# Optimization experiments

Hardware: AMD Instinct MI355X
Metric: run time of the kernel (lower is better)

The kernel has to match this reference:

```python
import jax, jax.numpy as jnp
import numpy as np

N_NODES = 100000
IN_CH, HID_CH, OUT_CH = 128, 256, 128
N_EDGES = 1600000


def setup_inputs() -> dict:
    key = jax.random.key(0)
    k_x, k_e, k_w1, k_b1, k_w2, k_b2 = jax.random.split(key, 6)
    x = jax.random.normal(k_x, (N_NODES, IN_CH), dtype=jnp.float32)
    edge_index = jax.random.randint(k_e, (2, N_EDGES), 0, N_NODES, dtype=jnp.int64)
    # MLP params (Linear stores weight [out,in]; we keep [in,out] for x @ W)
    lim1 = 1.0 / np.sqrt(IN_CH)
    lim2 = 1.0 / np.sqrt(HID_CH)
    W1 = jax.random.uniform(k_w1, (IN_CH, HID_CH), jnp.float32, -lim1, lim1)
    b1 = jax.random.uniform(k_b1, (HID_CH,), jnp.float32, -lim1, lim1)
    W2 = jax.random.uniform(k_w2, (HID_CH, OUT_CH), jnp.float32, -lim2, lim2)
    b2 = jax.random.uniform(k_b2, (OUT_CH,), jnp.float32, -lim2, lim2)
    eps = jnp.zeros((), jnp.float32)  # train_eps=True, init 0
    return {"x": x, "edge_index": edge_index, "W1": W1, "b1": b1,
            "W2": W2, "b2": b2, "eps": eps}


def reference(x, edge_index, W1, b1, W2, b2, eps):
    src, dst = edge_index[0], edge_index[1]
    # scatter-add neighbor aggregation: aggr[i] = sum_{(j->i)} x[j]
    aggr = jax.ops.segment_sum(x[src], dst, num_segments=N_NODES)  # [N, in]
    h = (1.0 + eps) * x + aggr
    h = jax.nn.relu(h @ W1 + b1)
    h = h @ W2 + b2
    h = jax.nn.relu(h)
    # dropout is identity in eval mode
    return jax.nn.log_softmax(h, axis=-1)
```

## Files before the change

### kernel.cpp

```cpp
#include <hip/hip_runtime.h>

#define N_NODES 100000
#define IN_CH 128
#define HID_CH 256
#define OUT_CH 128
#define N_EDGES 1600000

#define NBK 782
#define BIN_BLOCKS 256
#define EPB (N_EDGES / BIN_BLOCKS)

typedef __attribute__((ext_vector_type(8))) short short8;
typedef __attribute__((ext_vector_type(4))) float f32x4;

__device__ __forceinline__ float b2f(ushort u) {
    unsigned int x = ((unsigned int)u) << 16;
    return __uint_as_float(x);
}
__device__ __forceinline__ ushort f2b(float f) {
    unsigned int u = __float_as_uint(f);
    u += 0x7FFFu + ((u >> 16) & 1u);
    return (ushort)(u >> 16);
}

#define PREP_X_BLOCKS 6250
#define PREP_W1_BLOCKS 128
#define PREP_W2_BLOCKS 128
#define PREP_TOTAL (PREP_X_BLOCKS + PREP_W1_BLOCKS + PREP_W2_BLOCKS)
__global__ __launch_bounds__(256) void prep_kernel(
    const float* __restrict__ x, const float* __restrict__ W1,
    const float* __restrict__ W2, const int* __restrict__ dst,
    ushort* __restrict__ xb, ushort* __restrict__ W1T,
    ushort* __restrict__ W2T, int* __restrict__ histT) {
    const int b = blockIdx.x;
    const int t = threadIdx.x;
    if (b < PREP_X_BLOCKS) {
        const size_t i = (size_t)b * 2048 + t * 8;
        float4 a = *reinterpret_cast<const float4*>(x + i);
        float4 c = *reinterpret_cast<const float4*>(x + i + 4);
        ushort v[8] = {f2b(a.x), f2b(a.y), f2b(a.z), f2b(a.w),
                       f2b(c.x), f2b(c.y), f2b(c.z), f2b(c.w)};
        *reinterpret_cast<short8*>(xb + i) = *reinterpret_cast<short8*>(v);
    } else if (b < PREP_X_BLOCKS + PREP_W1_BLOCKS) {
        const int i = (b - PREP_X_BLOCKS) * 256 + t;
        const int oc = i >> 7, k = i & 127;
        W1T[i] = f2b(W1[k * HID_CH + oc]);
    } else if (b < PREP_TOTAL) {
        const int i = (b - PREP_X_BLOCKS - PREP_W1_BLOCKS) * 256 + t;
        const int oc = i >> 8, k = i & 255;
        W2T[i] = f2b(W2[k * OUT_CH + oc]);
    } else {
        __shared__ int h[NBK];
        const int bb = b - PREP_TOTAL;
        for (int k = t; k < NBK; k += 256) h[k] = 0;
        __syncthreads();
        const int base = bb * EPB;
        for (int i = t; i < EPB; i += 256)
            atomicAdd(&h[dst[base + i] >> 7], 1);
        __syncthreads();
        for (int k = t; k < NBK; k += 256) histT[k * BIN_BLOCKS + bb] = h[k];
    }
}

__global__ __launch_bounds__(256) void scanA_kernel(
    const int* __restrict__ histT, int* __restrict__ blockBaseP,
    int* __restrict__ bktTotal) {
    __shared__ int ts[256];
    const int bk = blockIdx.x, t = threadIdx.x;
    const int v = histT[bk * BIN_BLOCKS + t];
    ts[t] = v;
    __syncthreads();
    #pragma unroll
    for (int o = 1; o < 256; o <<= 1) {
        int add = (t >= o) ? ts[t - o] : 0;
        __syncthreads();
        ts[t] += add;
        __syncthreads();
    }
    blockBaseP[bk * BIN_BLOCKS + t] = ts[t] - v;
    if (t == 255) bktTotal[bk] = ts[255];
}

__global__ __launch_bounds__(1024) void scanB_kernel(
    const int* __restrict__ bktTotal, int* __restrict__ bktBase) {
    __shared__ int ts[1024];
    const int t = threadIdx.x;
    const int v = (t < NBK) ? bktTotal[t] : 0;
    ts[t] = v;
    __syncthreads();
    #pragma unroll
    for (int o = 1; o < 1024; o <<= 1) {
        int add = (t >= o) ? ts[t - o] : 0;
        __syncthreads();
        ts[t] += add;
        __syncthreads();
    }
    if (t < NBK) bktBase[t] = ts[t] - v;
}

__global__ __launch_bounds__(256) void bin_kernel(
    const int* __restrict__ src, const int* __restrict__ dst,
    const int* __restrict__ blockBaseP, const int* __restrict__ bktBase,
    unsigned int* __restrict__ ebuf) {
    __shared__ int base[NBK];
    __shared__ int cur[NBK];
    const int b = blockIdx.x, t = threadIdx.x;
    for (int k = t; k < NBK; k += 256) {
        base[k] = bktBase[k] + blockBaseP[k * BIN_BLOCKS + b];
        cur[k] = 0;
    }
    __syncthreads();
    const int ebase = b * EPB;
    for (int i = t; i < EPB; i += 256) {
        const int d = dst[ebase + i];
        const int s = src[ebase + i];
        const int bk = d >> 7;
        const int r = atomicAdd(&cur[bk], 1);
        ebuf[base[bk] + r] = ((unsigned int)(d & 127) << 17) | (unsigned int)s;
    }
}

__global__ __launch_bounds__(256) void group_kernel(
    const unsigned int* __restrict__ ebuf,
    const int* __restrict__ bktBase, const int* __restrict__ bktTotal,
    int* __restrict__ csr_src, int* __restrict__ offs) {
    __shared__ int hist[128];
    __shared__ int cur[128];
    const int bk = blockIdx.x, t = threadIdx.x;
    if (t < 128) hist[t] = 0;
    __syncthreads();
    const int start = bktBase[bk];
    const int cnt   = bktTotal[bk];
    for (int i = t; i < cnt; i += 256)
        atomicAdd(&hist[ebuf[start + i] >> 17], 1);
    __syncthreads();
    int v = (t < 128) ? hist[t] : 0;
    #pragma unroll
    for (int o = 1; o < 128; o <<= 1) {
        int add = (t < 128 && t >= o) ? hist[t - o] : 0;
        __syncthreads();
        if (t < 128) hist[t] += add;
        __syncthreads();
    }
    if (t < 128) {
        const int excl = hist[t] - v;
        cur[t] = excl;
        const int node = bk * 128 + t;
        if (node < N_NODES) offs[node] = start + excl;
    }
    if (bk == 0 && t == 0) offs[N_NODES] = N_EDGES;
    __syncthreads();
    for (int i = t; i < cnt; i += 256) {
        const unsigned int e = ebuf[start + i];
        const int dl = e >> 17;
        const int p = atomicAdd(&cur[dl], 1);
        csr_src[start + p] = (int)(e & 0x1FFFF);
    }
}

__global__ __launch_bounds__(256) void gather_kernel(
    const ushort* __restrict__ xb,
    const float* __restrict__ eps_p,
    const int* __restrict__ offs,
    const int* __restrict__ csr_src,
    ushort* __restrict__ h_in) {
    const int node = blockIdx.x * 4 + (threadIdx.x >> 6);
    const int l = threadIdx.x & 63;
    const int slice = l >> 4;
    const int c = (l & 15) * 8;
    const int beg = offs[node];
    const int end = offs[node + 1];

    float a0[8], a1[8];
    #pragma unroll
    for (int j = 0; j < 8; ++j) { a0[j] = 0.f; a1[j] = 0.f; }

    int base = beg;
    for (; base + 8 <= end; base += 8) {
        const int sidx = csr_src[base + (l & 7)];
        const int sA = __shfl(sidx, slice, 64);
        const int sB = __shfl(sidx, 4 + slice, 64);
        short8 vA = *reinterpret_cast<const short8*>(xb + (size_t)sA * IN_CH + c);
        short8 vB = *reinterpret_cast<const short8*>(xb + (size_t)sB * IN_CH + c);
        #pragma unroll
        for (int j = 0; j < 8; ++j) {
            a0[j] += b2f((ushort)vA[j]);
            a1[j] += b2f((ushort)vB[j]);
        }
    }
    const int r = end - base;
    if (r > 0) {
        const int sidx = csr_src[base + min(l & 7, r - 1)];
        const int sA = __shfl(sidx, min(slice, r - 1), 64);
        const int sB = __shfl(sidx, min(4 + slice, r - 1), 64);
        if (slice < r) {
            short8 vA = *reinterpret_cast<const short8*>(xb + (size_t)sA * IN_CH + c);
            #pragma unroll
            for (int j = 0; j < 8; ++j) a0[j] += b2f((ushort)vA[j]);
        }
        if (4 + slice < r) {
            short8 vB = *reinterpret_cast<const short8*>(xb + (size_t)sB * IN_CH + c);
            #pragma unroll
            for (int j = 0; j < 8; ++j) a1[j] += b2f((ushort)vB[j]);
        }
    }

    #pragma unroll
    for (int j = 0; j < 8; ++j) {
        a0[j] += a1[j];
        a0[j] += __shfl_xor(a0[j], 16, 64);
        a0[j] += __shfl_xor(a0[j], 32, 64);
    }

    if (l < 16) {
        const float scale = 1.0f + eps_p[0];
        short8 sv = *reinterpret_cast<const short8*>(xb + (size_t)node * IN_CH + c);
        ushort o[8];
        #pragma unroll
        for (int j = 0; j < 8; ++j)
            o[j] = f2b(scale * b2f((ushort)sv[j]) + a0[j]);
        *reinterpret_cast<short8*>(h_in + (size_t)node * IN_CH + c) =
            *reinterpret_cast<short8*>(o);
    }
}

#define H1_LD 264
__global__ __launch_bounds__(512) void mlp_fused(
    const ushort* __restrict__ h_in,
    const ushort* __restrict__ W1T,
    const ushort* __restrict__ W2T,
    const float* __restrict__ b1,
    const float* __restrict__ b2,
    float* __restrict__ out) {
    __shared__ ushort wbuf[32768];
    __shared__ ushort h1s[8][16 * H1_LD];
    const int t    = threadIdx.x;
    const int w    = t >> 6;
    const int lane = t & 63;
    const int lr   = lane & 15;
    const int lk   = lane >> 4;
    const int row0 = blockIdx.x * 128 + w * 16;
    const int arow = row0 + lr;
    const int arc  = arow < N_NODES ? arow : N_NODES - 1;
    ushort* tile = h1s[w];
    const int sw = (lr & 7) << 3;

    {
        const ushort* gw = W1T + t * 64;
        const int row = t >> 1;
        const int s = (row & 7) << 3;
        ushort* dstp = wbuf + row * 128;
        #pragma unroll
        for (int j = 0; j < 8; ++j) {
            short8 v = *reinterpret_cast<const short8*>(gw + j * 8);
            const int col = (t & 1) * 64 + j * 8;
            *reinterpret_cast<short8*>(dstp + (col ^ s)) = v;
        }
    }

    short8 a[4];
    const ushort* ap = h_in + (size_t)arc * IN_CH + lk * 8;
    #pragma unroll
    for (int kk = 0; kk < 4; ++kk)
        a[kk] = *reinterpret_cast<const short8*>(ap + kk * 32);

    __syncthreads();

    #pragma unroll
    for (int ct = 0; ct < 16; ++ct) {
        const ushort* bp = wbuf + (ct * 16 + lr) * 128;
        f32x4 acc = (f32x4){0.f, 0.f, 0.f, 0.f};
        #pragma unroll
        for (int kk = 0; kk < 4; ++kk) {
            short8 b = *reinterpret_cast<const short8*>(bp + ((lk * 8 + kk * 32) ^ sw));
            acc = __builtin_amdgcn_mfma_f32_16x16x32_bf16(a[kk], b, acc, 0, 0, 0);
        }
        const float bb = b1[ct * 16 + lr];
        #pragma unroll
        for (int r = 0; r < 4; ++r) {
            float v = fmaxf(acc[r] + bb, 0.0f);
            tile[(lk * 4 + r) * H1_LD + ct * 16 + lr] = f2b(v);
        }
    }

    __syncthreads();

    {
        const ushort* gw = W2T + t * 64;
        const int row = t >> 2;
        const int s = (row & 7) << 3;
        ushort* dstp = wbuf + row * 256;
        #pragma unroll
        for (int j = 0; j < 8; ++j) {
            short8 v = *reinterpret_cast<const short8*>(gw + j * 8);
            const int col = (t & 3) * 64 + j * 8;
            *reinterpret_cast<short8*>(dstp + (col ^ s)) = v;
        }
    }

    short8 a2[8];
    #pragma unroll
    for (int kk = 0; kk < 8; ++kk)
        a2[kk] = *reinterpret_cast<const short8*>(tile + lr * H1_LD + lk * 8 + kk * 32);

    __syncthreads();

    f32x4 acc2[8];
    #pragma unroll
    for (int ct = 0; ct < 8; ++ct) acc2[ct] = (f32x4){0.f, 0.f, 0.f, 0.f};

    #pragma unroll
    for (int ct = 0; ct < 8; ++ct) {
        const ushort* bp = wbuf + (ct * 16 + lr) * 256;
        #pragma unroll
        for (int kk = 0; kk < 8; ++kk) {
            short8 b = *reinterpret_cast<const short8*>(bp + ((lk * 8 + kk * 32) ^ sw));
            acc2[ct] = __builtin_amdgcn_mfma_f32_16x16x32_bf16(a2[kk], b, acc2[ct], 0, 0, 0);
        }
    }

    float bias[8];
    #pragma unroll
    for (int ct = 0; ct < 8; ++ct) bias[ct] = b2[ct * 16 + lr];

    const int orow0 = row0 + lk * 4;
    #pragma unroll
    for (int r = 0; r < 4; ++r) {
        float v[8];
        float m = -1e30f;
        #pragma unroll
        for (int ct = 0; ct < 8; ++ct) {
            v[ct] = fmaxf(acc2[ct][r] + bias[ct], 0.0f);
            m = fmaxf(m, v[ct]);
        }
        #pragma unroll
        for (int o = 1; o < 16; o <<= 1) m = fmaxf(m, __shfl_xor(m, o));
        float s = 0.0f;
        #pragma unroll
        for (int ct = 0; ct < 8; ++ct) s += __expf(v[ct] - m);
        #pragma unroll
        for (int o = 1; o < 16; o <<= 1) s += __shfl_xor(s, o);
        const float lse = m + __logf(s);
        const int orow = orow0 + r;
        if (orow < N_NODES) {
            #pragma unroll
            for (int ct = 0; ct < 8; ++ct)
                out[(size_t)orow * OUT_CH + ct * 16 + lr] = v[ct] - lse;
        }
    }
}

extern "C" void kernel_launch(void* const* d_in, const int* in_sizes, int n_in,
                              void* d_out, int out_size, void* d_ws, size_t ws_size,
                              hipStream_t stream) {
    const float* x    = (const float*)d_in[0];
    const int*   ei   = (const int*)d_in[1];
    const float* W1   = (const float*)d_in[2];
    const float* b1   = (const float*)d_in[3];
    const float* W2   = (const float*)d_in[4];
    const float* b2   = (const float*)d_in[5];
    const float* eps  = (const float*)d_in[6];
    float* out = (float*)d_out;

    ushort* xb   = (ushort*)d_ws;
    ushort* h_in = xb + (size_t)N_NODES * IN_CH;
    ushort* W1T  = h_in + (size_t)N_NODES * IN_CH;
    ushort* W2T  = W1T + IN_CH * HID_CH;
    int* histT      = (int*)(W2T + HID_CH * OUT_CH);
    int* blockBaseP = histT + NBK * BIN_BLOCKS;
    int* bktTotal   = blockBaseP + NBK * BIN_BLOCKS;
    int* bktBase    = bktTotal + NBK;
    int* offs       = bktBase + NBK;
    unsigned int* ebuf = (unsigned int*)(offs + N_NODES + 2);
    int* csr_src    = (int*)(ebuf + N_EDGES);

    const int* src = ei;
    const int* dst = ei + N_EDGES;

    prep_kernel<<<PREP_TOTAL + BIN_BLOCKS, 256, 0, stream>>>(
        x, W1, W2, dst, xb, W1T, W2T, histT);
    scanA_kernel<<<NBK, 256, 0, stream>>>(histT, blockBaseP, bktTotal);
    scanB_kernel<<<1, 1024, 0, stream>>>(bktTotal, bktBase);
    bin_kernel<<<BIN_BLOCKS, 256, 0, stream>>>(src, dst, blockBaseP, bktBase, ebuf);
    group_kernel<<<NBK, 256, 0, stream>>>(ebuf, bktBase, bktTotal, csr_src, offs);
    gather_kernel<<<N_NODES / 4, 256, 0, stream>>>(xb, eps, offs, csr_src, h_in);
    mlp_fused<<<(N_NODES + 127) / 128, 512, 0, stream>>>(h_in, W1T, W2T, b1, b2, out);
}
```

Baseline: 169.6 us.

## Keep hidden MLP activations in registers via lane shuffles instead of LDS

The first GEMM now computes the transposed product (weights as A operand), so each lane holds four consecutive hidden channels for one row. These are packed to bf16 pairs in registers and redistributed with cross-lane shuffles to form the A operand of the second GEMM, replacing the per-wave LDS staging tile. Dropping the tile cuts shared memory per block and a launch-bounds occupancy hint is added, at the cost of more registers and shuffle instructions. The bias load also becomes one vector load per lane.

```diff
diff --git a/kernel.cpp b/kernel.cpp
--- a/kernel.cpp
+++ b/kernel.cpp
@@ -224,8 +224,7 @@
     }
 }
 
-#define H1_LD 264
-__global__ __launch_bounds__(512) void mlp_fused(
+__global__ __launch_bounds__(512, 4) void mlp_fused(
     const ushort* __restrict__ h_in,
     const ushort* __restrict__ W1T,
     const ushort* __restrict__ W2T,
@@ -233,7 +232,6 @@
     const float* __restrict__ b2,
     float* __restrict__ out) {
     __shared__ ushort wbuf[32768];
-    __shared__ ushort h1s[8][16 * H1_LD];
     const int t    = threadIdx.x;
     const int w    = t >> 6;
     const int lane = t & 63;
@@ -242,7 +240,6 @@
     const int row0 = blockIdx.x * 128 + w * 16;
     const int arow = row0 + lr;
     const int arc  = arow < N_NODES ? arow : N_NODES - 1;
-    ushort* tile = h1s[w];
     const int sw = (lr & 7) << 3;
 
     {
@@ -266,21 +263,23 @@
 
     __syncthreads();
 
+    int pk[16][2];
     #pragma unroll
     for (int ct = 0; ct < 16; ++ct) {
         const ushort* bp = wbuf + (ct * 16 + lr) * 128;
         f32x4 acc = (f32x4){0.f, 0.f, 0.f, 0.f};
         #pragma unroll
         for (int kk = 0; kk < 4; ++kk) {
-            short8 b = *reinterpret_cast<const short8*>(bp + ((lk * 8 + kk * 32) ^ sw));
-            acc = __builtin_amdgcn_mfma_f32_16x16x32_bf16(a[kk], b, acc, 0, 0, 0);
-        }
-        const float bb = b1[ct * 16 + lr];
-        #pragma unroll
-        for (int r = 0; r < 4; ++r) {
-            float v = fmaxf(acc[r] + bb, 0.0f);
-            tile[(lk * 4 + r) * H1_LD + ct * 16 + lr] = f2b(v);
-        }
+            short8 wf = *reinterpret_cast<const short8*>(bp + ((lk * 8 + kk * 32) ^ sw));
+            acc = __builtin_amdgcn_mfma_f32_16x16x32_bf16(wf, a[kk], acc, 0, 0, 0);
+        }
+        const float4 bb = *reinterpret_cast<const float4*>(b1 + ct * 16 + lk * 4);
+        const float v0 = fmaxf(acc[0] + bb.x, 0.0f);
+        const float v1 = fmaxf(acc[1] + bb.y, 0.0f);
+        const float v2 = fmaxf(acc[2] + bb.z, 0.0f);
+        const float v3 = fmaxf(acc[3] + bb.w, 0.0f);
+        pk[ct][0] = (int)f2b(v0) | ((int)f2b(v1) << 16);
+        pk[ct][1] = (int)f2b(v2) | ((int)f2b(v3) << 16);
     }
 
     __syncthreads();
@@ -300,8 +299,19 @@
 
     short8 a2[8];
     #pragma unroll
-    for (int kk = 0; kk < 8; ++kk)
-        a2[kk] = *reinterpret_cast<const short8*>(tile + lr * H1_LD + lk * 8 + kk * 32);
+    for (int kk2 = 0; kk2 < 8; ++kk2) {
+        const int lo0 = pk[2 * kk2][0],     lo1 = pk[2 * kk2][1];
+        const int hi0 = pk[2 * kk2 + 1][0], hi1 = pk[2 * kk2 + 1][1];
+        union { int d[4]; short8 s8; } u;
+        #pragma unroll
+        for (int i = 0; i < 4; ++i) {
+            const int srcLane = lr + 16 * ((2 * lk + (i >> 1)) & 3);
+            const int vlo = __shfl((i & 1) ? lo1 : lo0, srcLane, 64);
+            const int vhi = __shfl((i & 1) ? hi1 : hi0, srcLane, 64);
+            u.d[i] = (lk < 2) ? vlo : vhi;
+        }
+        a2[kk2] = u.s8;
+    }
 
     __syncthreads();
 
```

Measured after the change: 163.5 us. 1.04x faster.
